# Performance work log

Measured on AMD Instinct MI355X. Metric: run time of the kernel, lower is better.

## Reference

```python
import jax, jax.numpy as jnp
import numpy as np

L, H, NH, F = 6, 1024, 16, 4096
B, S = 4, 512
D = H // NH
LN_EPS = 1e-12
GELU_C = 0.7978845608028654  # sqrt(2/pi)


def gelu_new(x):
    return 0.5 * x * (1.0 + jnp.tanh(GELU_C * (x + 0.044715 * x * x * x)))


def layer_norm(x, ln):
    # ln: [2, H] -> gamma, beta
    m = jnp.mean(x, axis=-1, keepdims=True)
    v = jnp.mean(jnp.square(x - m), axis=-1, keepdims=True)
    return (x - m) * jax.lax.rsqrt(v + LN_EPS) * ln[0] + ln[1]


def attention(q_in, kv_in, mask, qkv_w, qkv_b):
    # qkv_w: [3, H, H], qkv_b: [3, H]; mask: [B, S_kv] (1 = keep)
    b, s_q, _ = q_in.shape
    s_kv = kv_in.shape[1]
    q = (q_in @ qkv_w[0] + qkv_b[0]).reshape(b, s_q, NH, D)
    k = (kv_in @ qkv_w[1] + qkv_b[1]).reshape(b, s_kv, NH, D)
    v = (kv_in @ qkv_w[2] + qkv_b[2]).reshape(b, s_kv, NH, D)
    scale = 1.0 / (D ** 0.5)
    score = jnp.einsum('bind,bjnd->bnij', q, k) * scale  # [B, NH, Sq, Skv]
    adder = (1.0 - mask.astype(score.dtype))[:, None, None, :] * -10000.0
    prob = jax.nn.softmax(score + adder, axis=-1)
    out = jnp.einsum('bnij,bjnd->bind', prob, v)
    return out.reshape(b, s_q, H)


def _forward(hidden_states, encoder_hidden_states, attention_mask, encoder_attention_mask,
             sa_qkv_w, sa_qkv_b, sa_out_w, sa_out_b, sa_ln,
             ca_qkv_w, ca_qkv_b, ca_out_w, ca_out_b, ca_ln,
             o1_w, o1_b, o1_ln, ffn_w, ffn_b, o2_w, o2_b, o2_ln):
    h = hidden_states
    for i in range(L):
        # self attention + dense/dropout/LN (residual = h)
        self_vec = attention(h, h, attention_mask, sa_qkv_w[i], sa_qkv_b[i])
        attn_out = layer_norm(self_vec @ sa_out_w[i] + sa_out_b[i] + h, sa_ln[i])
        # cross attention + dense/dropout/LN (residual = h, per original code)
        cross_vec = attention(h, encoder_hidden_states, encoder_attention_mask,
                              ca_qkv_w[i], ca_qkv_b[i])
        cross_out = layer_norm(cross_vec @ ca_out_w[i] + ca_out_b[i] + h, ca_ln[i])
        # output_1: dense(attn_out) + cross_out, then LN
        attn_out = layer_norm(attn_out @ o1_w[i] + o1_b[i] + cross_out, o1_ln[i])
        # FFN with gelu_new, output_2: dense(inter) + attn_out, then LN
        inter = gelu_new(attn_out @ ffn_w[i] + ffn_b[i])
        h = layer_norm(inter @ o2_w[i] + o2_b[i] + attn_out, o2_ln[i])
    return h


def setup_inputs() -> dict:
    key = jax.random.key(0)
    ks = jax.random.split(key, 16)
    std = 0.02
    w = lambda k, shape: (jax.random.normal(k, shape, jnp.float32) * std)
    ln_init = jnp.stack([jnp.ones((L, H), jnp.float32), jnp.zeros((L, H), jnp.float32)], axis=1)
    return {
        'hidden_states': jax.random.normal(ks[0], (B, S, H), jnp.float32),
        'encoder_hidden_states': jax.random.normal(ks[1], (B, S, H), jnp.float32),
        'attention_mask': jnp.ones((B, S), jnp.int32),
        'encoder_attention_mask': jnp.ones((B, S), jnp.int32),
        'sa_qkv_w': w(ks[2], (L, 3, H, H)), 'sa_qkv_b': w(ks[3], (L, 3, H)),
        'sa_out_w': w(ks[4], (L, H, H)), 'sa_out_b': w(ks[5], (L, H)), 'sa_ln': ln_init,
        'ca_qkv_w': w(ks[6], (L, 3, H, H)), 'ca_qkv_b': w(ks[7], (L, 3, H)),
        'ca_out_w': w(ks[8], (L, H, H)), 'ca_out_b': w(ks[9], (L, H)), 'ca_ln': ln_init,
        'o1_w': w(ks[10], (L, H, H)), 'o1_b': w(ks[11], (L, H)), 'o1_ln': ln_init,
        'ffn_w': w(ks[12], (L, H, F)), 'ffn_b': w(ks[13], (L, F)),
        'o2_w': w(ks[14], (L, F, H)), 'o2_b': w(ks[15], (L, H)), 'o2_ln': ln_init,
    }


def reference(hidden_states, encoder_hidden_states, attention_mask, encoder_attention_mask,
              sa_qkv_w, sa_qkv_b, sa_out_w, sa_out_b, sa_ln,
              ca_qkv_w, ca_qkv_b, ca_out_w, ca_out_b, ca_ln,
              o1_w, o1_b, o1_ln, ffn_w, ffn_b, o2_w, o2_b, o2_ln):
    return _forward(hidden_states, encoder_hidden_states, attention_mask, encoder_attention_mask,
                    sa_qkv_w, sa_qkv_b, sa_out_w, sa_out_b, sa_ln,
                    ca_qkv_w, ca_qkv_b, ca_out_w, ca_out_b, ca_ln,
                    o1_w, o1_b, o1_ln, ffn_w, ffn_b, o2_w, o2_b, o2_ln)
```

## Files before the change

### kernel.cpp

```cpp
#include <hip/hip_runtime.h>


#define LNUM 6
#define HDIM 1024
#define NHEAD 16
#define DHEAD 64
#define BDIM 4
#define SDIM 512
#define FDIM 4096
#define MROWS (BDIM * SDIM)

typedef __bf16 bf16_t;
typedef bf16_t bf16x8 __attribute__((ext_vector_type(8)));
typedef float f32x4 __attribute__((ext_vector_type(4)));

__device__ __forceinline__ float bf2f(unsigned short u) {
    union { unsigned int i; float f; } x;
    x.i = ((unsigned int)u) << 16;
    return x.f;
}

__device__ __forceinline__ unsigned short f2bf(float f) {
    union { float f; unsigned int i; } u;
    u.f = f;
    unsigned int x = u.i;
    unsigned int lsb = (x >> 16) & 1u;
    x += 0x7fffu + lsb;
    return (unsigned short)(x >> 16);
}

__device__ __forceinline__ void async16(const unsigned short* g, unsigned short* l) {
    __builtin_amdgcn_global_load_lds(
        (const __attribute__((address_space(1))) unsigned int*)g,
        (__attribute__((address_space(3))) unsigned int*)l, 16, 0, 0);
}

template<int BM, int BN, bool GELU, bool OUTBF16>
__global__ __launch_bounds__(256) void mfma_gemm(
    const unsigned short* __restrict__ A,
    const unsigned short* __restrict__ BT,
    const float* __restrict__ bias,
    void* __restrict__ Cv,
    int M, int N, int K)
{
    constexpr int BK = 64;
    constexpr int MI = BM / 32;
    constexpr int NJ = BN / 32;

    __shared__ unsigned short As[2][BM][BK];
    __shared__ unsigned short Bs[2][BN][BK];

    const int t = threadIdx.x;
    const int w = t >> 6;
    const int lane = t & 63;
    const int quad = lane >> 4;
    const int cm = lane & 15;
    const int wrow = (w >> 1) * (BM / 2);
    const int wcol = (w & 1) * (BN / 2);
    const int row0 = blockIdx.x * BM;
    const int col0 = blockIdx.y * BN;

    f32x4 acc[MI][NJ] = {};

    const int lrow = lane >> 3;
    const int lcol = ((lane & 7) ^ lrow) * 8;
    const int sw = cm & 7;

    auto stage = [&](int buf, int k0) {
#pragma unroll
        for (int j = 0; j < BM / 32; ++j) {
            int mb = w * (BM / 4) + j * 8;
            async16(A + (size_t)(row0 + mb + lrow) * K + k0 + lcol, &As[buf][mb][0]);
        }
#pragma unroll
        for (int j = 0; j < BN / 32; ++j) {
            int nb = w * (BN / 4) + j * 8;
            async16(BT + (size_t)(col0 + nb + lrow) * K + k0 + lcol, &Bs[buf][nb][0]);
        }
    };

    stage(0, 0);
    __syncthreads();

    int cur = 0;
    for (int k0 = 0; k0 < K; k0 += BK) {
        if (k0 + BK < K) stage(cur ^ 1, k0 + BK);

#pragma unroll
        for (int kk = 0; kk < BK; kk += 32) {
            const int cc = kk >> 3;
            bf16x8 av[MI], bv[NJ];
#pragma unroll
            for (int i = 0; i < MI; ++i)
                av[i] = *(const bf16x8*)&As[cur][wrow + 16 * i + cm][((cc + quad) ^ sw) * 8];
#pragma unroll
            for (int j = 0; j < NJ; ++j)
                bv[j] = *(const bf16x8*)&Bs[cur][wcol + 16 * j + cm][((cc + quad) ^ sw) * 8];
#pragma unroll
            for (int i = 0; i < MI; ++i)
#pragma unroll
                for (int j = 0; j < NJ; ++j)
                    acc[i][j] = __builtin_amdgcn_mfma_f32_16x16x32_bf16(
                        av[i], bv[j], acc[i][j], 0, 0, 0);
        }
        __syncthreads();
        cur ^= 1;
    }

#pragma unroll
    for (int j = 0; j < NJ; ++j) {
        int col = col0 + wcol + 16 * j + cm;
        float bb = bias[col];
#pragma unroll
        for (int i = 0; i < MI; ++i) {
#pragma unroll
            for (int r = 0; r < 4; ++r) {
                int row = row0 + wrow + 16 * i + quad * 4 + r;
                float c = acc[i][j][r] + bb;
                if (GELU) {
                    float u = 0.7978845608028654f * (c + 0.044715f * c * c * c);
                    c = 0.5f * c * (1.0f + tanhf(u));
                }
                if (OUTBF16)
                    ((unsigned short*)Cv)[(size_t)row * N + col] = f2bf(c);
                else
                    ((float*)Cv)[(size_t)row * N + col] = c;
            }
        }
    }
}

template<int BM>
__global__ __launch_bounds__(256) void mfma_gemm_qkv(
    const unsigned short* __restrict__ Aq,
    const unsigned short* __restrict__ Akv,
    const unsigned short* __restrict__ BT,
    const float* __restrict__ bias,
    unsigned short* __restrict__ qo,
    unsigned short* __restrict__ ko,
    unsigned short* __restrict__ vo,
    int M, int K)
{
    constexpr int BK = 64;
    constexpr int BN = 64;
    constexpr int MI = BM / 32;
    constexpr int NJ = 2;

    __shared__ unsigned short As[2][BM][BK];
    __shared__ unsigned short Bs[2][BN][BK];

    const int t = threadIdx.x;
    const int w = t >> 6;
    const int lane = t & 63;
    const int quad = lane >> 4;
    const int cm = lane & 15;
    const int wrow = (w >> 1) * (BM / 2);
    const int wcol = (w & 1) * 32;
    const int row0 = blockIdx.x * BM;
    const int col0 = blockIdx.y * BN;

    const int which = col0 >> 10;
    const unsigned short* __restrict__ A = (which == 0) ? Aq : Akv;

    f32x4 acc[MI][NJ] = {};

    const int lrow = lane >> 3;
    const int lcol = ((lane & 7) ^ lrow) * 8;
    const int sw = cm & 7;

    auto stage = [&](int buf, int k0) {
#pragma unroll
        for (int j = 0; j < BM / 32; ++j) {
            int mb = w * (BM / 4) + j * 8;
            async16(A + (size_t)(row0 + mb + lrow) * K + k0 + lcol, &As[buf][mb][0]);
        }
#pragma unroll
        for (int j = 0; j < NJ; ++j) {
            int nb = w * 16 + j * 8;
            async16(BT + (size_t)(col0 + nb + lrow) * K + k0 + lcol, &Bs[buf][nb][0]);
        }
    };

    stage(0, 0);
    __syncthreads();

    int cur = 0;
    for (int k0 = 0; k0 < K; k0 += BK) {
        if (k0 + BK < K) stage(cur ^ 1, k0 + BK);

#pragma unroll
        for (int kk = 0; kk < BK; kk += 32) {
            const int cc = kk >> 3;
            bf16x8 av[MI], bv[NJ];
#pragma unroll
            for (int i = 0; i < MI; ++i)
                av[i] = *(const bf16x8*)&As[cur][wrow + 16 * i + cm][((cc + quad) ^ sw) * 8];
#pragma unroll
            for (int j = 0; j < NJ; ++j)
                bv[j] = *(const bf16x8*)&Bs[cur][wcol + 16 * j + cm][((cc + quad) ^ sw) * 8];
#pragma unroll
            for (int i = 0; i < MI; ++i)
#pragma unroll
                for (int j = 0; j < NJ; ++j)
                    acc[i][j] = __builtin_amdgcn_mfma_f32_16x16x32_bf16(
                        av[i], bv[j], acc[i][j], 0, 0, 0);
        }
        __syncthreads();
        cur ^= 1;
    }

    unsigned short* dst = (which == 0) ? qo : (which == 1) ? ko : vo;
    const int cbase = col0 & 1023;

#pragma unroll
    for (int j = 0; j < NJ; ++j) {
        int col = col0 + wcol + 16 * j + cm;
        float bb = bias[col];
        int coll = cbase + wcol + 16 * j + cm;
#pragma unroll
        for (int i = 0; i < MI; ++i) {
#pragma unroll
            for (int r = 0; r < 4; ++r) {
                int row = row0 + wrow + 16 * i + quad * 4 + r;
                dst[(size_t)row * HDIM + coll] = f2bf(acc[i][j][r] + bb);
            }
        }
    }
}

__global__ __launch_bounds__(256) void flash_attn(
    const unsigned short* __restrict__ q,
    const unsigned short* __restrict__ k,
    const unsigned short* __restrict__ v,
    const int* __restrict__ mask,
    unsigned short* __restrict__ ctx)
{
    __shared__ unsigned short Qs[64][64];
    __shared__ unsigned short Ks[64][64];
    __shared__ unsigned short Vs[64][72];
    __shared__ unsigned short Ps[4][16][72];

    const int t = threadIdx.x;
    const int w = t >> 6;
    const int lane = t & 63;
    const int quad = lane >> 4;
    const int cm = lane & 15;
    const int sw = cm & 7;

    const int q0 = blockIdx.x * 64;
    const int h = blockIdx.y;
    const int b = blockIdx.z;
    const size_t rowbase = (size_t)b * SDIM;
    const int hoff = h * DHEAD;

#pragma unroll
    for (int l = 0; l < 2; ++l) {
        int idx = t + l * 256;
        int r = idx >> 3;
        int c = idx & 7;
        *(uint4*)&Qs[r][((c ^ (r & 7)) * 8)] =
            *(const uint4*)(q + (rowbase + q0 + r) * HDIM + hoff + c * 8);
    }

    float m_prev[4] = {-1e30f, -1e30f, -1e30f, -1e30f};
    float l_sum[4] = {0.0f, 0.0f, 0.0f, 0.0f};
    f32x4 oacc[4] = {};

    for (int j0 = 0; j0 < SDIM; j0 += 64) {
        __syncthreads();
#pragma unroll
        for (int l = 0; l < 2; ++l) {
            int idx = t + l * 256;
            int r = idx >> 3;
            int c = idx & 7;
            *(uint4*)&Ks[r][((c ^ (r & 7)) * 8)] =
                *(const uint4*)(k + (rowbase + j0 + r) * HDIM + hoff + c * 8);
        }
#pragma unroll
        for (int l = 0; l < 4; ++l) {
            int idx = t + l * 256;
            int jj = idx >> 4;
            int d0 = (idx & 15) * 4;
            ushort4 vv = *(const ushort4*)(v + (rowbase + j0 + jj) * HDIM + hoff + d0);
            Vs[d0 + 0][jj] = vv.x;
            Vs[d0 + 1][jj] = vv.y;
            Vs[d0 + 2][jj] = vv.z;
            Vs[d0 + 3][jj] = vv.w;
        }
        __syncthreads();

        f32x4 sacc[4] = {};
#pragma unroll
        for (int kk = 0; kk < 64; kk += 32) {
            const int cc = kk >> 3;
            bf16x8 av = *(const bf16x8*)&Qs[w * 16 + cm][((cc + quad) ^ sw) * 8];
#pragma unroll
            for (int j2 = 0; j2 < 4; ++j2) {
                bf16x8 bv = *(const bf16x8*)&Ks[j2 * 16 + cm][((cc + quad) ^ sw) * 8];
                sacc[j2] = __builtin_amdgcn_mfma_f32_16x16x32_bf16(av, bv, sacc[j2], 0, 0, 0);
            }
        }

        float madd[4];
#pragma unroll
        for (int j2 = 0; j2 < 4; ++j2)
            madd[j2] = (1.0f - (float)mask[b * SDIM + j0 + j2 * 16 + cm]) * -10000.0f;

#pragma unroll
        for (int r = 0; r < 4; ++r) {
            float s0 = sacc[0][r] * 0.125f + madd[0];
            float s1 = sacc[1][r] * 0.125f + madd[1];
            float s2 = sacc[2][r] * 0.125f + madd[2];
            float s3 = sacc[3][r] * 0.125f + madd[3];
            float rm = fmaxf(fmaxf(s0, s1), fmaxf(s2, s3));
#pragma unroll
            for (int mo = 1; mo < 16; mo <<= 1)
                rm = fmaxf(rm, __shfl_xor(rm, mo, 64));
            float new_m = fmaxf(m_prev[r], rm);
            float alpha = __expf(m_prev[r] - new_m);
            m_prev[r] = new_m;
            float p0 = __expf(s0 - new_m);
            float p1 = __expf(s1 - new_m);
            float p2 = __expf(s2 - new_m);
            float p3 = __expf(s3 - new_m);
            float rs = p0 + p1 + p2 + p3;
#pragma unroll
            for (int mo = 1; mo < 16; mo <<= 1)
                rs += __shfl_xor(rs, mo, 64);
            l_sum[r] = l_sum[r] * alpha + rs;
#pragma unroll
            for (int d2 = 0; d2 < 4; ++d2)
                oacc[d2][r] *= alpha;
            int prow = quad * 4 + r;
            Ps[w][prow][0 * 16 + cm] = f2bf(p0);
            Ps[w][prow][1 * 16 + cm] = f2bf(p1);
            Ps[w][prow][2 * 16 + cm] = f2bf(p2);
            Ps[w][prow][3 * 16 + cm] = f2bf(p3);
        }

#pragma unroll
        for (int kk = 0; kk < 64; kk += 32) {
            bf16x8 pa = *(const bf16x8*)&Ps[w][cm][kk + quad * 8];
#pragma unroll
            for (int d2 = 0; d2 < 4; ++d2) {
                bf16x8 bv = *(const bf16x8*)&Vs[d2 * 16 + cm][kk + quad * 8];
                oacc[d2] = __builtin_amdgcn_mfma_f32_16x16x32_bf16(pa, bv, oacc[d2], 0, 0, 0);
            }
        }
    }

#pragma unroll
    for (int r = 0; r < 4; ++r) {
        float inv = 1.0f / l_sum[r];
        int row = q0 + w * 16 + quad * 4 + r;
#pragma unroll
        for (int d2 = 0; d2 < 4; ++d2) {
            ctx[(rowbase + row) * HDIM + hoff + d2 * 16 + cm] = f2bf(oacc[d2][r] * inv);
        }
    }
}

__global__ __launch_bounds__(256) void convtrans_kernel(
    const float* __restrict__ in, unsigned short* __restrict__ out, int K, int N)
{
    __shared__ unsigned short tile[64][72];
    const size_t moff = (size_t)blockIdx.z * K * N;
    const int n0 = blockIdx.x * 64, k0 = blockIdx.y * 64;
    const int t = threadIdx.x;
#pragma unroll
    for (int l = 0; l < 4; ++l) {
        int idx = t + l * 256;
        int kk = idx >> 4;
        int nn = (idx & 15) * 4;
        float4 v = *(const float4*)(in + moff + (size_t)(k0 + kk) * N + n0 + nn);
        tile[nn + 0][kk] = f2bf(v.x);
        tile[nn + 1][kk] = f2bf(v.y);
        tile[nn + 2][kk] = f2bf(v.z);
        tile[nn + 3][kk] = f2bf(v.w);
    }
    __syncthreads();
#pragma unroll
    for (int l = 0; l < 2; ++l) {
        int c = t + l * 256;
        int nn = c >> 3;
        int kk = (c & 7) * 8;
        *(uint4*)(out + moff + (size_t)(n0 + nn) * K + k0 + kk) =
            *(const uint4*)&tile[nn][kk];
    }
}

template<bool OUTF32>
__global__ __launch_bounds__(256) void ln_kernel(
    const float* __restrict__ x, const unsigned short* __restrict__ resid,
    const float* __restrict__ ln, void* __restrict__ out)
{
    const int row = blockIdx.x;
    const float* xr = x + (size_t)row * HDIM;
    const unsigned short* rr = resid + (size_t)row * HDIM;
    const int t = threadIdx.x;
    __shared__ float red[4];

    float4 xv = ((const float4*)xr)[t];
    ushort4 rv = ((const ushort4*)rr)[t];
    float z[4];
    z[0] = xv.x + bf2f(rv.x);
    z[1] = xv.y + bf2f(rv.y);
    z[2] = xv.z + bf2f(rv.z);
    z[3] = xv.w + bf2f(rv.w);
    float s = z[0] + z[1] + z[2] + z[3];
#pragma unroll
    for (int off = 32; off > 0; off >>= 1) s += __shfl_down(s, off, 64);
    if ((t & 63) == 0) red[t >> 6] = s;
    __syncthreads();
    s = red[0] + red[1] + red[2] + red[3];
    float mean = s * (1.0f / (float)HDIM);

    float vs = 0.0f;
#pragma unroll
    for (int i = 0; i < 4; ++i) {
        float d = z[i] - mean;
        vs += d * d;
    }
#pragma unroll
    for (int off = 32; off > 0; off >>= 1) vs += __shfl_down(vs, off, 64);
    __syncthreads();
    if ((t & 63) == 0) red[t >> 6] = vs;
    __syncthreads();
    vs = red[0] + red[1] + red[2] + red[3];
    float inv = rsqrtf(vs * (1.0f / (float)HDIM) + 1e-12f);

    const float* g = ln + 4 * t;
    const float* bb = ln + HDIM + 4 * t;
    if (OUTF32) {
        float4 o;
        o.x = (z[0] - mean) * inv * g[0] + bb[0];
        o.y = (z[1] - mean) * inv * g[1] + bb[1];
        o.z = (z[2] - mean) * inv * g[2] + bb[2];
        o.w = (z[3] - mean) * inv * g[3] + bb[3];
        ((float4*)((float*)out + (size_t)row * HDIM))[t] = o;
    } else {
        ushort4 o;
        o.x = f2bf((z[0] - mean) * inv * g[0] + bb[0]);
        o.y = f2bf((z[1] - mean) * inv * g[1] + bb[1]);
        o.z = f2bf((z[2] - mean) * inv * g[2] + bb[2]);
        o.w = f2bf((z[3] - mean) * inv * g[3] + bb[3]);
        ((ushort4*)((unsigned short*)out + (size_t)row * HDIM))[t] = o;
    }
}

__global__ __launch_bounds__(256) void cvt_bf16_kernel(
    const float* __restrict__ in, unsigned short* __restrict__ out, int n4)
{
    int i = blockIdx.x * 256 + threadIdx.x;
    if (i < n4) {
        float4 v = ((const float4*)in)[i];
        ushort4 o;
        o.x = f2bf(v.x); o.y = f2bf(v.y); o.z = f2bf(v.z); o.w = f2bf(v.w);
        ((ushort4*)out)[i] = o;
    }
}

extern "C" void kernel_launch(void* const* d_in, const int* in_sizes, int n_in,
                              void* d_out, int out_size, void* d_ws, size_t ws_size,
                              hipStream_t stream)
{
    const float* in_hidden = (const float*)d_in[0];
    const float* enc_f     = (const float*)d_in[1];
    const int* attn_mask   = (const int*)d_in[2];
    const int* enc_attn_mask = (const int*)d_in[3];
    const float* sa_qkv_w  = (const float*)d_in[4];
    const float* sa_qkv_b  = (const float*)d_in[5];
    const float* sa_out_w  = (const float*)d_in[6];
    const float* sa_out_b  = (const float*)d_in[7];
    const float* sa_ln     = (const float*)d_in[8];
    const float* ca_qkv_w  = (const float*)d_in[9];
    const float* ca_qkv_b  = (const float*)d_in[10];
    const float* ca_out_w  = (const float*)d_in[11];
    const float* ca_out_b  = (const float*)d_in[12];
    const float* ca_ln     = (const float*)d_in[13];
    const float* o1_w      = (const float*)d_in[14];
    const float* o1_b      = (const float*)d_in[15];
    const float* o1_ln     = (const float*)d_in[16];
    const float* ffn_w     = (const float*)d_in[17];
    const float* ffn_b     = (const float*)d_in[18];
    const float* o2_w      = (const float*)d_in[19];
    const float* o2_b      = (const float*)d_in[20];
    const float* o2_ln     = (const float*)d_in[21];

    const size_t MH  = (size_t)MROWS * HDIM;
    const size_t Hsq = (size_t)HDIM * HDIM;
    const size_t HF  = (size_t)HDIM * FDIM;

    char* p = (char*)d_ws;
    unsigned short* wbf = (unsigned short*)p; p += (9 * Hsq + 2 * HF) * 2;
    float* t2     = (float*)p; p += MH * 4;
    unsigned short* qb     = (unsigned short*)p; p += MH * 2;
    unsigned short* kb     = (unsigned short*)p; p += MH * 2;
    unsigned short* vb     = (unsigned short*)p; p += MH * 2;
    unsigned short* ctx    = (unsigned short*)p; p += MH * 2;
    unsigned short* h      = (unsigned short*)p; p += MH * 2;
    unsigned short* enc_bf = (unsigned short*)p; p += MH * 2;
    unsigned short* attn1  = (unsigned short*)p; p += MH * 2;
    unsigned short* crossb = (unsigned short*)p; p += MH * 2;
    unsigned short* attn2  = (unsigned short*)p; p += MH * 2;
    unsigned short* tmp8b  = (unsigned short*)p; p += (size_t)MROWS * FDIM * 2;

    unsigned short* w_saqkv = wbf;
    unsigned short* w_saout = wbf + 3 * Hsq;
    unsigned short* w_caqkv = wbf + 4 * Hsq;
    unsigned short* w_caout = wbf + 7 * Hsq;
    unsigned short* w_o1    = wbf + 8 * Hsq;
    unsigned short* w_ffn   = wbf + 9 * Hsq;
    unsigned short* w_o2    = wbf + 9 * Hsq + HF;

    cvt_bf16_kernel<<<(MH / 4 + 255) / 256, 256, 0, stream>>>(in_hidden, h, MH / 4);
    cvt_bf16_kernel<<<(MH / 4 + 255) / 256, 256, 0, stream>>>(enc_f, enc_bf, MH / 4);

    for (int l = 0; l < LNUM; ++l) {
        convtrans_kernel<<<dim3(HDIM / 64, HDIM / 64, 3), 256, 0, stream>>>(
            sa_qkv_w + (size_t)l * 3 * Hsq, w_saqkv, HDIM, HDIM);
        convtrans_kernel<<<dim3(HDIM / 64, HDIM / 64, 1), 256, 0, stream>>>(
            sa_out_w + (size_t)l * Hsq, w_saout, HDIM, HDIM);
        convtrans_kernel<<<dim3(HDIM / 64, HDIM / 64, 3), 256, 0, stream>>>(
            ca_qkv_w + (size_t)l * 3 * Hsq, w_caqkv, HDIM, HDIM);
        convtrans_kernel<<<dim3(HDIM / 64, HDIM / 64, 1), 256, 0, stream>>>(
            ca_out_w + (size_t)l * Hsq, w_caout, HDIM, HDIM);
        convtrans_kernel<<<dim3(HDIM / 64, HDIM / 64, 1), 256, 0, stream>>>(
            o1_w + (size_t)l * Hsq, w_o1, HDIM, HDIM);
        convtrans_kernel<<<dim3(FDIM / 64, HDIM / 64, 1), 256, 0, stream>>>(
            ffn_w + (size_t)l * HF, w_ffn, HDIM, FDIM);
        convtrans_kernel<<<dim3(HDIM / 64, FDIM / 64, 1), 256, 0, stream>>>(
            o2_w + (size_t)l * HF, w_o2, FDIM, HDIM);

        mfma_gemm_qkv<64><<<dim3(MROWS / 64, 3072 / 64), 256, 0, stream>>>(
            h, h, w_saqkv, sa_qkv_b + (size_t)l * 3 * HDIM, qb, kb, vb, MROWS, HDIM);
        flash_attn<<<dim3(SDIM / 64, NHEAD, BDIM), 256, 0, stream>>>(
            qb, kb, vb, attn_mask, ctx);
        mfma_gemm<64, 64, false, false><<<dim3(MROWS / 64, HDIM / 64), 256, 0, stream>>>(
            ctx, w_saout, sa_out_b + (size_t)l * HDIM, t2, MROWS, HDIM, HDIM);
        ln_kernel<false><<<MROWS, 256, 0, stream>>>(t2, h, sa_ln + (size_t)l * 2 * HDIM, attn1);

        mfma_gemm_qkv<64><<<dim3(MROWS / 64, 3072 / 64), 256, 0, stream>>>(
            h, enc_bf, w_caqkv, ca_qkv_b + (size_t)l * 3 * HDIM, qb, kb, vb, MROWS, HDIM);
        flash_attn<<<dim3(SDIM / 64, NHEAD, BDIM), 256, 0, stream>>>(
            qb, kb, vb, enc_attn_mask, ctx);
        mfma_gemm<64, 64, false, false><<<dim3(MROWS / 64, HDIM / 64), 256, 0, stream>>>(
            ctx, w_caout, ca_out_b + (size_t)l * HDIM, t2, MROWS, HDIM, HDIM);
        ln_kernel<false><<<MROWS, 256, 0, stream>>>(t2, h, ca_ln + (size_t)l * 2 * HDIM, crossb);

        mfma_gemm<64, 64, false, false><<<dim3(MROWS / 64, HDIM / 64), 256, 0, stream>>>(
            attn1, w_o1, o1_b + (size_t)l * HDIM, t2, MROWS, HDIM, HDIM);
        ln_kernel<false><<<MROWS, 256, 0, stream>>>(t2, crossb, o1_ln + (size_t)l * 2 * HDIM, attn2);

        mfma_gemm<128, 128, true, true><<<dim3(MROWS / 128, FDIM / 128), 256, 0, stream>>>(
            attn2, w_ffn, ffn_b + (size_t)l * FDIM, tmp8b, MROWS, FDIM, HDIM);
        mfma_gemm<64, 64, false, false><<<dim3(MROWS / 64, HDIM / 64), 256, 0, stream>>>(
            tmp8b, w_o2, o2_b + (size_t)l * HDIM, t2, MROWS, HDIM, FDIM);
        if (l == LNUM - 1)
            ln_kernel<true><<<MROWS, 256, 0, stream>>>(
                t2, attn2, o2_ln + (size_t)l * 2 * HDIM, (float*)d_out);
        else
            ln_kernel<false><<<MROWS, 256, 0, stream>>>(
                t2, attn2, o2_ln + (size_t)l * 2 * HDIM, h);
    }
}
```

Baseline: 2.069 ms.

## Use explicit vmcnt waits in GEMM loop, merge weight conversions, retile FFN

The GEMM main loops now issue the next tile's async LDS loads, wait on vmcnt only for the current tile, and use raw s_barrier with sched_barrier fences instead of __syncthreads. This lets prefetch stay in flight across the barrier. The seven per-layer weight convert/transpose launches become a single kernel that dispatches on a flat block index, cutting launch overhead. The FFN up-projection tile shrinks from 128x128 to 64x128 to launch more blocks. The hand-written waitcnt logic depends on the exact number of loads issued per thread, so a wrong count could produce LDS races.

```diff
diff --git a/kernel.cpp b/kernel.cpp
--- a/kernel.cpp
+++ b/kernel.cpp
@@ -9,6 +9,7 @@
 #define SDIM 512
 #define FDIM 4096
 #define MROWS (BDIM * SDIM)
+#define HSQ (HDIM * HDIM)
 
 typedef __bf16 bf16_t;
 typedef bf16_t bf16x8 __attribute__((ext_vector_type(8)));
@@ -33,6 +34,11 @@
     __builtin_amdgcn_global_load_lds(
         (const __attribute__((address_space(1))) unsigned int*)g,
         (__attribute__((address_space(3))) unsigned int*)l, 16, 0, 0);
+}
+
+template<int N>
+__device__ __forceinline__ void s_wait_vmcnt() {
+    asm volatile("s_waitcnt vmcnt(%0)" :: "n"(N) : "memory");
 }
 
 template<int BM, int BN, bool GELU, bool OUTBF16>
@@ -46,6 +52,7 @@
     constexpr int BK = 64;
     constexpr int MI = BM / 32;
     constexpr int NJ = BN / 32;
+    constexpr int LPT = BM / 32 + BN / 32;
 
     __shared__ unsigned short As[2][BM][BK];
     __shared__ unsigned short Bs[2][BN][BK];
@@ -79,12 +86,18 @@
         }
     };
 
+    const int NT = K / BK;
     stage(0, 0);
-    __syncthreads();
-
     int cur = 0;
-    for (int k0 = 0; k0 < K; k0 += BK) {
-        if (k0 + BK < K) stage(cur ^ 1, k0 + BK);
+    for (int ti = 0; ti < NT; ++ti) {
+        if (ti + 1 < NT) {
+            stage(cur ^ 1, (ti + 1) * BK);
+            s_wait_vmcnt<LPT>();
+        } else {
+            s_wait_vmcnt<0>();
+        }
+        __builtin_amdgcn_s_barrier();
+        __builtin_amdgcn_sched_barrier(0);
 
 #pragma unroll
         for (int kk = 0; kk < BK; kk += 32) {
@@ -103,7 +116,9 @@
                     acc[i][j] = __builtin_amdgcn_mfma_f32_16x16x32_bf16(
                         av[i], bv[j], acc[i][j], 0, 0, 0);
         }
-        __syncthreads();
+
+        __builtin_amdgcn_sched_barrier(0);
+        __builtin_amdgcn_s_barrier();
         cur ^= 1;
     }
 
@@ -145,6 +160,7 @@
     constexpr int BN = 64;
     constexpr int MI = BM / 32;
     constexpr int NJ = 2;
+    constexpr int LPT = BM / 32 + BN / 32;
 
     __shared__ unsigned short As[2][BM][BK];
     __shared__ unsigned short Bs[2][BN][BK];
@@ -181,12 +197,18 @@
         }
     };
 
+    const int NT = K / BK;
     stage(0, 0);
-    __syncthreads();
-
     int cur = 0;
-    for (int k0 = 0; k0 < K; k0 += BK) {
-        if (k0 + BK < K) stage(cur ^ 1, k0 + BK);
+    for (int ti = 0; ti < NT; ++ti) {
+        if (ti + 1 < NT) {
+            stage(cur ^ 1, (ti + 1) * BK);
+            s_wait_vmcnt<LPT>();
+        } else {
+            s_wait_vmcnt<0>();
+        }
+        __builtin_amdgcn_s_barrier();
+        __builtin_amdgcn_sched_barrier(0);
 
 #pragma unroll
         for (int kk = 0; kk < BK; kk += 32) {
@@ -205,7 +227,9 @@
                     acc[i][j] = __builtin_amdgcn_mfma_f32_16x16x32_bf16(
                         av[i], bv[j], acc[i][j], 0, 0, 0);
         }
-        __syncthreads();
+
+        __builtin_amdgcn_sched_barrier(0);
+        __builtin_amdgcn_s_barrier();
         cur ^= 1;
     }
 
@@ -360,19 +384,45 @@
     }
 }
 
-__global__ __launch_bounds__(256) void convtrans_kernel(
-    const float* __restrict__ in, unsigned short* __restrict__ out, int K, int N)
+__global__ __launch_bounds__(256) void convtrans_all(
+    const float* __restrict__ sqkv, const float* __restrict__ sout,
+    const float* __restrict__ cqkv, const float* __restrict__ cout,
+    const float* __restrict__ o1w,  const float* __restrict__ ffnw,
+    const float* __restrict__ o2w,
+    unsigned short* __restrict__ dq,  unsigned short* __restrict__ dso,
+    unsigned short* __restrict__ dcq, unsigned short* __restrict__ dco,
+    unsigned short* __restrict__ do1, unsigned short* __restrict__ dffn,
+    unsigned short* __restrict__ do2)
 {
     __shared__ unsigned short tile[64][72];
-    const size_t moff = (size_t)blockIdx.z * K * N;
-    const int n0 = blockIdx.x * 64, k0 = blockIdx.y * 64;
+    const int bid = blockIdx.x;
+    const float* src;
+    unsigned short* dst;
+    int K, N, tt;
+    if (bid < 2304) {
+        int m = bid >> 8;
+        tt = bid & 255;
+        K = HDIM; N = HDIM;
+        if (m < 3)      { src = sqkv + (size_t)m * HSQ;       dst = dq  + (size_t)m * HSQ; }
+        else if (m < 6) { src = cqkv + (size_t)(m - 3) * HSQ; dst = dcq + (size_t)(m - 3) * HSQ; }
+        else if (m == 6){ src = sout; dst = dso; }
+        else if (m == 7){ src = cout; dst = dco; }
+        else            { src = o1w;  dst = do1; }
+    } else if (bid < 3328) {
+        tt = bid - 2304; K = HDIM; N = FDIM; src = ffnw; dst = dffn;
+    } else {
+        tt = bid - 3328; K = FDIM; N = HDIM; src = o2w; dst = do2;
+    }
+    const int tn = N >> 6;
+    const int n0 = (tt % tn) * 64;
+    const int k0 = (tt / tn) * 64;
     const int t = threadIdx.x;
 #pragma unroll
     for (int l = 0; l < 4; ++l) {
         int idx = t + l * 256;
         int kk = idx >> 4;
         int nn = (idx & 15) * 4;
-        float4 v = *(const float4*)(in + moff + (size_t)(k0 + kk) * N + n0 + nn);
+        float4 v = *(const float4*)(src + (size_t)(k0 + kk) * N + n0 + nn);
         tile[nn + 0][kk] = f2bf(v.x);
         tile[nn + 1][kk] = f2bf(v.y);
         tile[nn + 2][kk] = f2bf(v.z);
@@ -384,8 +434,7 @@
         int c = t + l * 256;
         int nn = c >> 3;
         int kk = (c & 7) * 8;
-        *(uint4*)(out + moff + (size_t)(n0 + nn) * K + k0 + kk) =
-            *(const uint4*)&tile[nn][kk];
+        *(uint4*)(dst + (size_t)(n0 + nn) * K + k0 + kk) = *(const uint4*)&tile[nn][kk];
     }
 }
 
@@ -517,20 +566,11 @@
     cvt_bf16_kernel<<<(MH / 4 + 255) / 256, 256, 0, stream>>>(enc_f, enc_bf, MH / 4);
 
     for (int l = 0; l < LNUM; ++l) {
-        convtrans_kernel<<<dim3(HDIM / 64, HDIM / 64, 3), 256, 0, stream>>>(
-            sa_qkv_w + (size_t)l * 3 * Hsq, w_saqkv, HDIM, HDIM);
-        convtrans_kernel<<<dim3(HDIM / 64, HDIM / 64, 1), 256, 0, stream>>>(
-            sa_out_w + (size_t)l * Hsq, w_saout, HDIM, HDIM);
-        convtrans_kernel<<<dim3(HDIM / 64, HDIM / 64, 3), 256, 0, stream>>>(
-            ca_qkv_w + (size_t)l * 3 * Hsq, w_caqkv, HDIM, HDIM);
-        convtrans_kernel<<<dim3(HDIM / 64, HDIM / 64, 1), 256, 0, stream>>>(
-            ca_out_w + (size_t)l * Hsq, w_caout, HDIM, HDIM);
-        convtrans_kernel<<<dim3(HDIM / 64, HDIM / 64, 1), 256, 0, stream>>>(
-            o1_w + (size_t)l * Hsq, w_o1, HDIM, HDIM);
-        convtrans_kernel<<<dim3(FDIM / 64, HDIM / 64, 1), 256, 0, stream>>>(
-            ffn_w + (size_t)l * HF, w_ffn, HDIM, FDIM);
-        convtrans_kernel<<<dim3(HDIM / 64, FDIM / 64, 1), 256, 0, stream>>>(
-            o2_w + (size_t)l * HF, w_o2, FDIM, HDIM);
+        convtrans_all<<<4352, 256, 0, stream>>>(
+            sa_qkv_w + (size_t)l * 3 * Hsq, sa_out_w + (size_t)l * Hsq,
+            ca_qkv_w + (size_t)l * 3 * Hsq, ca_out_w + (size_t)l * Hsq,
+            o1_w + (size_t)l * Hsq, ffn_w + (size_t)l * HF, o2_w + (size_t)l * HF,
+            w_saqkv, w_saout, w_caqkv, w_caout, w_o1, w_ffn, w_o2);
 
         mfma_gemm_qkv<64><<<dim3(MROWS / 64, 3072 / 64), 256, 0, stream>>>(
             h, h, w_saqkv, sa_qkv_b + (size_t)l * 3 * HDIM, qb, kb, vb, MROWS, HDIM);
@@ -552,7 +592,7 @@
             attn1, w_o1, o1_b + (size_t)l * HDIM, t2, MROWS, HDIM, HDIM);
         ln_kernel<false><<<MROWS, 256, 0, stream>>>(t2, crossb, o1_ln + (size_t)l * 2 * HDIM, attn2);
 
-        mfma_gemm<128, 128, true, true><<<dim3(MROWS / 128, FDIM / 128), 256, 0, stream>>>(
+        mfma_gemm<64, 128, true, true><<<dim3(MROWS / 64, FDIM / 128), 256, 0, stream>>>(
             attn2, w_ffn, ffn_b + (size_t)l * FDIM, tmp8b, MROWS, FDIM, HDIM);
         mfma_gemm<64, 64, false, false><<<dim3(MROWS / 64, HDIM / 64), 256, 0, stream>>>(
             tmp8b, w_o2, o2_b + (size_t)l * HDIM, t2, MROWS, HDIM, FDIM);
```

New measurement: 2.012 ms. 1.03x faster.
